# Kernel optimization log

Measured on AMD Instinct MI355X. Metric: run time of the kernel, lower is better.

The kernel has to match this reference:

```python
import jax, jax.numpy as jnp
import numpy as np

B, S, D = 2, 2048, 1024
H, DK = 16, 64


def setup_inputs() -> dict:
    key = jax.random.key(0)
    ks = jax.random.split(key, 10)
    scale = D ** -0.5
    x = jax.random.normal(ks[0], (B, S, D), dtype=jnp.float32)
    mask = jax.random.randint(ks[1], (B, S), 0, 2) > 0  # True = masked positions
    Wq = jax.random.normal(ks[2], (D, H * DK), dtype=jnp.float32) * scale
    Wk = jax.random.normal(ks[3], (D, H * DK), dtype=jnp.float32) * scale
    Wv = jax.random.normal(ks[4], (D, H * DK), dtype=jnp.float32) * scale
    Wo = jax.random.normal(ks[5], (H * DK, D), dtype=jnp.float32) * scale
    bq = jnp.zeros((H * DK,), jnp.float32)
    bk = jnp.zeros((H * DK,), jnp.float32)
    bv = jnp.zeros((H * DK,), jnp.float32)
    bo = jnp.zeros((D,), jnp.float32)
    return {"x": x, "mask": mask, "Wq": Wq, "bq": bq, "Wk": Wk, "bk": bk,
            "Wv": Wv, "bv": bv, "Wo": Wo, "bo": bo}


def reference(x, mask, Wq, bq, Wk, bk, Wv, bv, Wo, bo):
    b, s, _ = x.shape
    # Linear + activation (dropout is identity at eval)
    q = jax.nn.relu(x @ Wq + bq).reshape(b, s, H, DK)
    k = jax.nn.relu(x @ Wk + bk).reshape(b, s, H, DK)
    v = jax.nn.relu(x @ Wv + bv).reshape(b, s, H, DK)
    # scores: [B, H, Sq, Sk]
    attn = jnp.einsum("bqhd,bkhd->bhqk", q, k) * (DK ** -0.5)
    # NOTE: original uses masked_fill(mask, 1e-9) BEFORE softmax (not -inf)
    attn = jnp.where(mask[:, None, None, :], jnp.float32(1e-9), attn)
    attn = jax.nn.softmax(attn, axis=-1)
    out = jnp.einsum("bhqk,bkhd->bqhd", attn, v).reshape(b, s, H * DK)
    return jax.nn.relu(out @ Wo + bo)
```

## Files before the change

### kernel.cpp

```cpp
#include <hip/hip_runtime.h>
#include <stdint.h>

typedef __attribute__((ext_vector_type(8))) short short8;
typedef __attribute__((ext_vector_type(4))) short short4b;
typedef __attribute__((ext_vector_type(4))) float f32x4;
typedef __attribute__((ext_vector_type(4))) unsigned short ushort4_t;

#define MFMA16(a, b, c) __builtin_amdgcn_mfma_f32_16x16x32_bf16((a), (b), (c), 0, 0, 0)

#if defined(__HIP_DEVICE_COMPILE__)
  #if __has_builtin(__builtin_amdgcn_mfma_f32_16x16x16bf16_1k)
    #define MFMA16K16(a, b, c) __builtin_amdgcn_mfma_f32_16x16x16bf16_1k((a), (b), (c), 0, 0, 0)
  #else
    #define MFMA16K16(a, b, c) __builtin_amdgcn_mfma_f32_16x16x16_bf16((a), (b), (c), 0, 0, 0)
  #endif
#else
  #define MFMA16K16(a, b, c) (c)
#endif

#define SCL_F (0.125f * 1.44269504f)

__device__ __forceinline__ float b2f(unsigned short u) {
    union { unsigned u; float f; } c; c.u = ((unsigned)u) << 16; return c.f;
}
__device__ __forceinline__ unsigned short f2b(float f) {
    union { float f; unsigned u; } c; c.f = f;
    unsigned r = c.u + 0x7FFF + ((c.u >> 16) & 1);
    return (unsigned short)(r >> 16);
}
__device__ __forceinline__ unsigned f_as_u(float f) {
    union { float f; unsigned u; } c; c.f = f; return c.u;
}

__device__ __forceinline__ void g2lds16(const unsigned short* g, unsigned lds_byte_off) {
    __builtin_amdgcn_global_load_lds(
        (const __attribute__((address_space(1))) void*)(uintptr_t)g,
        (__attribute__((address_space(3))) void*)(uintptr_t)lds_byte_off,
        16, 0, 0);
}

__global__ void detect_dtype(const unsigned short* __restrict__ x, int* __restrict__ flag) {
    __shared__ int cnt;
    if (threadIdx.x == 0) cnt = 0;
    __syncthreads();
    int insane = 0;
    #pragma unroll
    for (int j = 0; j < 4; ++j) {
        unsigned short u = x[threadIdx.x * 4 + j];
        int e = (u >> 7) & 0xFF;
        if ((e >= 1 && e <= 90) || e >= 165) insane++;
    }
    atomicAdd(&cnt, insane);
    __syncthreads();
    if (threadIdx.x == 0) *flag = (cnt > 128) ? 1 : 0;
}

__global__ __launch_bounds__(256) void convtrans_k(const void* __restrict__ s0, const void* __restrict__ s1,
                                                   const void* __restrict__ s2, const void* __restrict__ s3,
                                                   const void* __restrict__ b0, const void* __restrict__ b1,
                                                   const void* __restrict__ b2, const void* __restrict__ b3s,
                                                   const void* __restrict__ xsrc,
                                                   unsigned short* __restrict__ xdst,
                                                   unsigned short* __restrict__ dstBase,
                                                   unsigned short* __restrict__ dstB3,
                                                   unsigned short* __restrict__ dstBo,
                                                   const int* __restrict__ flag) {
    const int z = blockIdx.z;
    if (z >= 5) {
        if (!*flag) return;
        const int slice = z - 5;
        const size_t i0 = (size_t)slice * 524288 + (blockIdx.y * 16 + blockIdx.x) * 2048 + threadIdx.x * 8;
        const float* s = (const float*)xsrc;
        float4 f0 = *(const float4*)&s[i0];
        float4 f1 = *(const float4*)&s[i0 + 4];
        unsigned short* t = &xdst[i0];
        t[0] = f2b(f0.x); t[1] = f2b(f0.y); t[2] = f2b(f0.z); t[3] = f2b(f0.w);
        t[4] = f2b(f1.x); t[5] = f2b(f1.y); t[6] = f2b(f1.z); t[7] = f2b(f1.w);
        return;
    }
    if (z == 4) {
        if (blockIdx.y != 0 || blockIdx.x >= 4) return;
        const int w = blockIdx.x;
        const void* src = (w == 0) ? b0 : (w == 1) ? b1 : (w == 2) ? b2 : b3s;
        const float bscl = (w == 0) ? SCL_F : 1.0f;
        #pragma unroll
        for (int j = 0; j < 4; ++j) {
            const int i = threadIdx.x * 4 + j;
            float fv = (*flag) ? ((const float*)src)[i] : b2f(((const unsigned short*)src)[i]);
            unsigned short v = f2b(fv * bscl);
            if (w < 3) dstB3[w * 1024 + i] = v;
            else dstBo[i] = v;
        }
        return;
    }
    __shared__ __align__(16) unsigned short tile[64 * 72];
    const void* src = (z == 0) ? s0 : (z == 1) ? s1 : (z == 2) ? s2 : s3;
    unsigned short* dst = dstBase + (size_t)z * 1024 * 1024;
    const float wscl = (z == 0) ? SCL_F : 1.0f;
    const int tid = threadIdx.x;
    const int r0 = blockIdx.y * 64, c0 = blockIdx.x * 64;
    const int rb = tid >> 3, c = (tid & 7) * 8;
    if (*flag) {
        const float* s = (const float*)src;
        #pragma unroll
        for (int it = 0; it < 2; ++it) {
            int rr = it * 32 + rb;
            float4 f0 = *(const float4*)&s[(size_t)(r0 + rr) * 1024 + c0 + c];
            float4 f1 = *(const float4*)&s[(size_t)(r0 + rr) * 1024 + c0 + c + 4];
            unsigned short* t = &tile[rr * 72 + c];
            t[0] = f2b(f0.x * wscl); t[1] = f2b(f0.y * wscl); t[2] = f2b(f0.z * wscl); t[3] = f2b(f0.w * wscl);
            t[4] = f2b(f1.x * wscl); t[5] = f2b(f1.y * wscl); t[6] = f2b(f1.z * wscl); t[7] = f2b(f1.w * wscl);
        }
    } else if (z == 0) {
        const unsigned short* s = (const unsigned short*)src;
        #pragma unroll
        for (int it = 0; it < 2; ++it) {
            int rr = it * 32 + rb;
            union { short8 v; unsigned short u[8]; } in;
            in.v = *(const short8*)&s[(size_t)(r0 + rr) * 1024 + c0 + c];
            unsigned short* t = &tile[rr * 72 + c];
            #pragma unroll
            for (int j = 0; j < 8; ++j) t[j] = f2b(b2f(in.u[j]) * SCL_F);
        }
    } else {
        const unsigned short* s = (const unsigned short*)src;
        #pragma unroll
        for (int it = 0; it < 2; ++it) {
            int rr = it * 32 + rb;
            *(short8*)&tile[rr * 72 + c] = *(const short8*)&s[(size_t)(r0 + rr) * 1024 + c0 + c];
        }
    }
    __syncthreads();
    #pragma unroll
    for (int it = 0; it < 2; ++it) {
        int n = it * 32 + rb, k8 = c;
        union { short8 s; unsigned short u[8]; } tmp;
        #pragma unroll
        for (int j = 0; j < 8; ++j) tmp.u[j] = tile[(k8 + j) * 72 + n];
        *(short8*)&dst[(size_t)(c0 + n) * 1024 + r0 + k8] = tmp.s;
    }
}

__global__ __launch_bounds__(256) void mask_k(unsigned short* __restrict__ qkv,
                                              const int* __restrict__ mask) {
    const int row = blockIdx.x * 2 + (threadIdx.x >> 7);
    const int col = (threadIdx.x & 127) * 8;
    if (mask[row]) {
        const short8 z = {0, 0, 0, 0, 0, 0, 0, 0};
        *(short8*)&qkv[(size_t)row * 3072 + 1024 + col] = z;
    }
}

__global__ __launch_bounds__(256) void gemm_bias_relu(const unsigned short* __restrict__ A,
                                                      const void* __restrict__ Araw,
                                                      const unsigned short* __restrict__ BT,
                                                      const unsigned short* __restrict__ bias,
                                                      void* __restrict__ C,
                                                      unsigned short* __restrict__ VtG,
                                                      const int* __restrict__ flag,
                                                      int M, int N, int K, int mode) {
    __shared__ __align__(16) unsigned short As[128 * 32];
    __shared__ __align__(16) unsigned short Bs[128 * 32];
    const int tid = threadIdx.x;
    const int wave = tid >> 6, lane = tid & 63;
    const int quad = lane >> 4, l16 = lane & 15;
    const int wm = wave >> 1, wn = wave & 1;
    const int m0 = blockIdx.y * 128, n0 = blockIdx.x * 128;

    const unsigned short* Ause = (Araw != nullptr && *flag == 0) ? (const unsigned short*)Araw : A;

    f32x4 acc[4][4];
    #pragma unroll
    for (int i = 0; i < 4; i++)
        #pragma unroll
        for (int j = 0; j < 4; j++) acc[i][j] = (f32x4){0.f, 0.f, 0.f, 0.f};

    const int srow = wave * 32 + (lane >> 2);
    const int sc8  = (lane & 3) * 8;
    const unsigned short* gA0 = Ause + (size_t)(m0 + srow) * K + sc8;
    const unsigned short* gA1 = gA0 + (size_t)16 * K;
    const unsigned short* gB0 = BT + (size_t)(n0 + srow) * K + sc8;
    const unsigned short* gB1 = gB0 + (size_t)16 * K;
    const unsigned ldsA = (unsigned)(uintptr_t)&As[0] + wave * 2048;
    const unsigned ldsB = (unsigned)(uintptr_t)&Bs[0] + wave * 2048;

    for (int k0 = 0; k0 < K; k0 += 32) {
        __syncthreads();
        g2lds16(gA0 + k0, ldsA);
        g2lds16(gA1 + k0, ldsA + 1024);
        g2lds16(gB0 + k0, ldsB);
        g2lds16(gB1 + k0, ldsB + 1024);
        __syncthreads();
        short8 af[4], bf[4];
        #pragma unroll
        for (int i = 0; i < 4; i++) af[i] = *(const short8*)&As[(wm * 64 + i * 16 + l16) * 32 + quad * 8];
        #pragma unroll
        for (int j = 0; j < 4; j++) bf[j] = *(const short8*)&Bs[(wn * 64 + j * 16 + l16) * 32 + quad * 8];
        #pragma unroll
        for (int i = 0; i < 4; i++)
            #pragma unroll
            for (int j = 0; j < 4; j++)
                acc[i][j] = MFMA16(af[i], bf[j], acc[i][j]);
    }

    if (mode == 2 && n0 >= 2048) {
        #pragma unroll
        for (int j = 0; j < 4; j++) {
            const int col = n0 + wn * 64 + j * 16 + l16;
            const int h  = (col - 2048) >> 6;
            const int dk = (col - 2048) & 63;
            const float bj = b2f(bias[col]);
            #pragma unroll
            for (int i = 0; i < 4; i++) {
                const int rowb = m0 + wm * 64 + i * 16 + quad * 4;
                const int bb = rowb >> 11;
                const int s0 = rowb & 2047;
                ushort4_t w;
                #pragma unroll
                for (int r = 0; r < 4; r++) {
                    float v = acc[i][j][r] + bj;
                    v = v > 0.f ? v : 0.f;
                    w[r] = f2b(v);
                }
                *(ushort4_t*)&VtG[(size_t)((bb * 16 + h) * 64 + dk) * 2048 + s0] = w;
            }
        }
    } else {
        const int f32out = (mode == 1) && (*flag != 0);
        #pragma unroll
        for (int j = 0; j < 4; j++) {
            const int col = n0 + wn * 64 + j * 16 + l16;
            const float bj = b2f(bias[col]);
            #pragma unroll
            for (int i = 0; i < 4; i++) {
                const int rowb = m0 + wm * 64 + i * 16 + quad * 4;
                #pragma unroll
                for (int r = 0; r < 4; r++) {
                    float v = acc[i][j][r] + bj;
                    v = v > 0.f ? v : 0.f;
                    if (f32out) ((float*)C)[(size_t)(rowb + r) * N + col] = v;
                    else ((unsigned short*)C)[(size_t)(rowb + r) * N + col] = f2b(v);
                }
            }
        }
    }
}

__global__ __launch_bounds__(256) void attn_kernel(const unsigned short* __restrict__ qkv,
                                                   const unsigned short* __restrict__ VtG,
                                                   unsigned short* __restrict__ out) {
    __shared__ __align__(16) unsigned short Ks[64 * 64];
    __shared__ __align__(16) unsigned short Vs[64 * 64];

    const int qt = blockIdx.x, bh = blockIdx.y;
    const int b = bh >> 4, h = bh & 15;
    const int tid = threadIdx.x, wave = tid >> 6, lane = tid & 63;
    const int quad = lane >> 4, l16 = lane & 15;

    const int qrowA = qt * 128 + wave * 16 + l16;
    const unsigned short* qpA = qkv + (size_t)(b * 2048 + qrowA) * 3072 + h * 64;
    const unsigned short* qpB = qpA + (size_t)64 * 3072;
    const short8 qa0 = *(const short8*)(qpA + quad * 8);
    const short8 qa1 = *(const short8*)(qpA + 32 + quad * 8);
    const short8 qb0 = *(const short8*)(qpB + quad * 8);
    const short8 qb1 = *(const short8*)(qpB + 32 + quad * 8);

    f32x4 oA[4], oB[4], sumA, sumB;
    #pragma unroll
    for (int n = 0; n < 4; n++) { oA[n] = (f32x4){0.f,0.f,0.f,0.f}; oB[n] = (f32x4){0.f,0.f,0.f,0.f}; }
    sumA = (f32x4){0.f,0.f,0.f,0.f};
    sumB = (f32x4){0.f,0.f,0.f,0.f};

    const short4b ones = { (short)0x3F80, (short)0x3F80, (short)0x3F80, (short)0x3F80 };

    const int srow = tid >> 2;
    const int scol = (tid & 3) * 16;
    const int sxor = (srow & 7) << 3;
    const unsigned short* kg = qkv + (size_t)(b * 2048 + srow) * 3072 + 1024 + h * 64 + scol;
    const unsigned short* vg = VtG + (size_t)(bh * 64 + srow) * 2048 + scol;
    const size_t kstep = (size_t)64 * 3072;
    unsigned short* wK0 = &Ks[(srow * 64 + scol) ^ sxor];
    unsigned short* wK1 = &Ks[(srow * 64 + scol + 8) ^ sxor];
    unsigned short* wV0 = &Vs[(srow * 64 + scol) ^ sxor];
    unsigned short* wV1 = &Vs[(srow * 64 + scol + 8) ^ sxor];

    const int rx = (l16 & 7) << 3;

    short8 rk0 = *(const short8*)(kg);
    short8 rk1 = *(const short8*)(kg + 8);
    short8 rv0 = *(const short8*)(vg);
    short8 rv1 = *(const short8*)(vg + 8);

    for (int kt = 0; kt < 32; ++kt) {
        __syncthreads();
        *(short8*)wK0 = rk0;
        *(short8*)wK1 = rk1;
        *(short8*)wV0 = rv0;
        *(short8*)wV1 = rv1;
        if (kt < 31) {
            rk0 = *(const short8*)(kg + (kt + 1) * kstep);
            rk1 = *(const short8*)(kg + (kt + 1) * kstep + 8);
            rv0 = *(const short8*)(vg + (kt + 1) * 64);
            rv1 = *(const short8*)(vg + (kt + 1) * 64 + 8);
        }
        __syncthreads();

        __builtin_amdgcn_s_setprio(1);
        f32x4 sA[4], sB[4];
        #pragma unroll
        for (int t = 0; t < 4; ++t) {
            const short8 kb0 = *(const short8*)&Ks[(((t * 16 + l16) * 64) + quad * 8) ^ rx];
            const short8 kb1 = *(const short8*)&Ks[(((t * 16 + l16) * 64) + 32 + quad * 8) ^ rx];
            f32x4 z = (f32x4){0.f, 0.f, 0.f, 0.f};
            sA[t] = MFMA16(kb1, qa1, MFMA16(kb0, qa0, z));
            sB[t] = MFMA16(kb1, qb1, MFMA16(kb0, qb0, z));
        }

        short4b vb[4][4];
        #pragma unroll
        for (int t = 0; t < 4; ++t)
            #pragma unroll
            for (int n = 0; n < 4; ++n)
                vb[t][n] = *(const short4b*)&Vs[(((n * 16 + l16) * 64) + t * 16 + quad * 4) ^ rx];

        #pragma unroll
        for (int t = 0; t < 4; ++t) {
            float pA[4], pB[4];
            #pragma unroll
            for (int r = 0; r < 4; ++r) {
                pA[r] = exp2f(sA[t][r]);
                pB[r] = exp2f(sB[t][r]);
            }
            union { unsigned u[2]; short4b s; } fa, fb;
            fa.u[0] = __builtin_amdgcn_perm(f_as_u(pA[1]), f_as_u(pA[0]), 0x07060302u);
            fa.u[1] = __builtin_amdgcn_perm(f_as_u(pA[3]), f_as_u(pA[2]), 0x07060302u);
            fb.u[0] = __builtin_amdgcn_perm(f_as_u(pB[1]), f_as_u(pB[0]), 0x07060302u);
            fb.u[1] = __builtin_amdgcn_perm(f_as_u(pB[3]), f_as_u(pB[2]), 0x07060302u);
            #pragma unroll
            for (int n = 0; n < 4; ++n) {
                oA[n] = MFMA16K16(fa.s, vb[t][n], oA[n]);
                oB[n] = MFMA16K16(fb.s, vb[t][n], oB[n]);
            }
            sumA = MFMA16K16(fa.s, ones, sumA);
            sumB = MFMA16K16(fb.s, ones, sumB);
        }
        __builtin_amdgcn_s_setprio(0);
    }

    float invA[4], invB[4];
    #pragma unroll
    for (int r = 0; r < 4; ++r) { invA[r] = 1.0f / sumA[r]; invB[r] = 1.0f / sumB[r]; }
    #pragma unroll
    for (int n = 0; n < 4; n++)
        #pragma unroll
        for (int r = 0; r < 4; r++) {
            const int row = qt * 128 + wave * 16 + quad * 4 + r;
            out[(size_t)(b * 2048 + row) * 1024 + h * 64 + n * 16 + l16] = f2b(oA[n][r] * invA[r]);
            out[(size_t)(b * 2048 + row + 64) * 1024 + h * 64 + n * 16 + l16] = f2b(oB[n][r] * invB[r]);
        }
}

extern "C" void kernel_launch(void* const* d_in, const int* in_sizes, int n_in,
                              void* d_out, int out_size, void* d_ws, size_t ws_size,
                              hipStream_t stream) {
    const void* x  = d_in[0];
    const int*  mk = (const int*)d_in[1];
    const void* Wq = d_in[2]; const void* bq = d_in[3];
    const void* Wk = d_in[4]; const void* bk = d_in[5];
    const void* Wv = d_in[6]; const void* bv = d_in[7];
    const void* Wo = d_in[8]; const void* bo = d_in[9];

    char* wsb = (char*)d_ws;
    int* flag = (int*)wsb;
    unsigned short* W0 = (unsigned short*)(wsb + 64);

    const size_t M1 = 1024u * 1024u;
    const size_t M4 = 4096u * 1024u;
    unsigned short* xb  = W0;
    unsigned short* WT  = xb + M4;
    unsigned short* WoT = WT + 3 * M1;
    unsigned short* b3  = WoT + M1;
    unsigned short* bob = b3 + 4096;
    unsigned short* qkv = bob + 1024;
    unsigned short* VtG = qkv + (size_t)4096 * 3072;
    unsigned short* abf = xb;

    detect_dtype<<<1, 256, 0, stream>>>((const unsigned short*)x, flag);

    convtrans_k<<<dim3(16, 16, 13), 256, 0, stream>>>(Wq, Wk, Wv, Wo, bq, bk, bv, bo,
                                                      x, xb, WT, b3, bob, flag);

    gemm_bias_relu<<<dim3(24, 32), 256, 0, stream>>>(xb, x, WT, b3, qkv, VtG, flag,
                                                     4096, 3072, 1024, 2);
    mask_k<<<2048, 256, 0, stream>>>(qkv, mk);
    attn_kernel<<<dim3(16, 32), 256, 0, stream>>>(qkv, VtG, abf);
    gemm_bias_relu<<<dim3(8, 32), 256, 0, stream>>>(abf, nullptr, WoT, bob, d_out, VtG, flag,
                                                    4096, 1024, 1024, 1);
}
```

Measured before the change: 227.2 us.

## Halve attention query tile and double-buffer K/V shared memory

The attention kernel now processes 64 query rows per block instead of 128 and launches twice as many blocks, giving 1024 workgroups instead of 512 to fill the GPU's compute units. K/V tiles are double-buffered in LDS, so each iteration needs one barrier instead of two, and the global loads for the next tile are issued two iterations ahead. The cost is that every K/V tile is loaded from global memory twice as many times overall, and LDS use per block doubles.

```diff
diff --git a/kernel.cpp b/kernel.cpp
--- a/kernel.cpp
+++ b/kernel.cpp
@@ -249,27 +249,23 @@
 __global__ __launch_bounds__(256) void attn_kernel(const unsigned short* __restrict__ qkv,
                                                    const unsigned short* __restrict__ VtG,
                                                    unsigned short* __restrict__ out) {
-    __shared__ __align__(16) unsigned short Ks[64 * 64];
-    __shared__ __align__(16) unsigned short Vs[64 * 64];
+    __shared__ __align__(16) unsigned short Ks[2][64 * 64];
+    __shared__ __align__(16) unsigned short Vs[2][64 * 64];
 
     const int qt = blockIdx.x, bh = blockIdx.y;
     const int b = bh >> 4, h = bh & 15;
     const int tid = threadIdx.x, wave = tid >> 6, lane = tid & 63;
     const int quad = lane >> 4, l16 = lane & 15;
 
-    const int qrowA = qt * 128 + wave * 16 + l16;
-    const unsigned short* qpA = qkv + (size_t)(b * 2048 + qrowA) * 3072 + h * 64;
-    const unsigned short* qpB = qpA + (size_t)64 * 3072;
-    const short8 qa0 = *(const short8*)(qpA + quad * 8);
-    const short8 qa1 = *(const short8*)(qpA + 32 + quad * 8);
-    const short8 qb0 = *(const short8*)(qpB + quad * 8);
-    const short8 qb1 = *(const short8*)(qpB + 32 + quad * 8);
-
-    f32x4 oA[4], oB[4], sumA, sumB;
-    #pragma unroll
-    for (int n = 0; n < 4; n++) { oA[n] = (f32x4){0.f,0.f,0.f,0.f}; oB[n] = (f32x4){0.f,0.f,0.f,0.f}; }
+    const int qrow = qt * 64 + wave * 16 + l16;
+    const unsigned short* qp = qkv + (size_t)(b * 2048 + qrow) * 3072 + h * 64;
+    const short8 qa0 = *(const short8*)(qp + quad * 8);
+    const short8 qa1 = *(const short8*)(qp + 32 + quad * 8);
+
+    f32x4 oA[4], sumA;
+    #pragma unroll
+    for (int n = 0; n < 4; n++) oA[n] = (f32x4){0.f,0.f,0.f,0.f};
     sumA = (f32x4){0.f,0.f,0.f,0.f};
-    sumB = (f32x4){0.f,0.f,0.f,0.f};
 
     const short4b ones = { (short)0x3F80, (short)0x3F80, (short)0x3F80, (short)0x3F80 };
 
@@ -279,41 +275,50 @@
     const unsigned short* kg = qkv + (size_t)(b * 2048 + srow) * 3072 + 1024 + h * 64 + scol;
     const unsigned short* vg = VtG + (size_t)(bh * 64 + srow) * 2048 + scol;
     const size_t kstep = (size_t)64 * 3072;
-    unsigned short* wK0 = &Ks[(srow * 64 + scol) ^ sxor];
-    unsigned short* wK1 = &Ks[(srow * 64 + scol + 8) ^ sxor];
-    unsigned short* wV0 = &Vs[(srow * 64 + scol) ^ sxor];
-    unsigned short* wV1 = &Vs[(srow * 64 + scol + 8) ^ sxor];
+    const int sidx0 = (srow * 64 + scol) ^ sxor;
+    const int sidx1 = (srow * 64 + scol + 8) ^ sxor;
 
     const int rx = (l16 & 7) << 3;
+
+    unsigned short* Ka = &Ks[0][0];  unsigned short* Kb = &Ks[1][0];
+    unsigned short* Va = &Vs[0][0];  unsigned short* Vb = &Vs[1][0];
 
     short8 rk0 = *(const short8*)(kg);
     short8 rk1 = *(const short8*)(kg + 8);
     short8 rv0 = *(const short8*)(vg);
     short8 rv1 = *(const short8*)(vg + 8);
+    *(short8*)(Ka + sidx0) = rk0;
+    *(short8*)(Ka + sidx1) = rk1;
+    *(short8*)(Va + sidx0) = rv0;
+    *(short8*)(Va + sidx1) = rv1;
+    rk0 = *(const short8*)(kg + kstep);
+    rk1 = *(const short8*)(kg + kstep + 8);
+    rv0 = *(const short8*)(vg + 64);
+    rv1 = *(const short8*)(vg + 64 + 8);
+    __syncthreads();
 
     for (int kt = 0; kt < 32; ++kt) {
-        __syncthreads();
-        *(short8*)wK0 = rk0;
-        *(short8*)wK1 = rk1;
-        *(short8*)wV0 = rv0;
-        *(short8*)wV1 = rv1;
         if (kt < 31) {
-            rk0 = *(const short8*)(kg + (kt + 1) * kstep);
-            rk1 = *(const short8*)(kg + (kt + 1) * kstep + 8);
-            rv0 = *(const short8*)(vg + (kt + 1) * 64);
-            rv1 = *(const short8*)(vg + (kt + 1) * 64 + 8);
-        }
-        __syncthreads();
+            *(short8*)(Kb + sidx0) = rk0;
+            *(short8*)(Kb + sidx1) = rk1;
+            *(short8*)(Vb + sidx0) = rv0;
+            *(short8*)(Vb + sidx1) = rv1;
+        }
+        if (kt < 30) {
+            rk0 = *(const short8*)(kg + (kt + 2) * kstep);
+            rk1 = *(const short8*)(kg + (kt + 2) * kstep + 8);
+            rv0 = *(const short8*)(vg + (kt + 2) * 64);
+            rv1 = *(const short8*)(vg + (kt + 2) * 64 + 8);
+        }
 
         __builtin_amdgcn_s_setprio(1);
-        f32x4 sA[4], sB[4];
+        f32x4 sA[4];
         #pragma unroll
         for (int t = 0; t < 4; ++t) {
-            const short8 kb0 = *(const short8*)&Ks[(((t * 16 + l16) * 64) + quad * 8) ^ rx];
-            const short8 kb1 = *(const short8*)&Ks[(((t * 16 + l16) * 64) + 32 + quad * 8) ^ rx];
+            const short8 kb0 = *(const short8*)&Ka[(((t * 16 + l16) * 64) + quad * 8) ^ rx];
+            const short8 kb1 = *(const short8*)&Ka[(((t * 16 + l16) * 64) + 32 + quad * 8) ^ rx];
             f32x4 z = (f32x4){0.f, 0.f, 0.f, 0.f};
             sA[t] = MFMA16(kb1, qa1, MFMA16(kb0, qa0, z));
-            sB[t] = MFMA16(kb1, qb1, MFMA16(kb0, qb0, z));
         }
 
         short4b vb[4][4];
@@ -321,42 +326,38 @@
         for (int t = 0; t < 4; ++t)
             #pragma unroll
             for (int n = 0; n < 4; ++n)
-                vb[t][n] = *(const short4b*)&Vs[(((n * 16 + l16) * 64) + t * 16 + quad * 4) ^ rx];
+                vb[t][n] = *(const short4b*)&Va[(((n * 16 + l16) * 64) + t * 16 + quad * 4) ^ rx];
 
         #pragma unroll
         for (int t = 0; t < 4; ++t) {
-            float pA[4], pB[4];
-            #pragma unroll
-            for (int r = 0; r < 4; ++r) {
-                pA[r] = exp2f(sA[t][r]);
-                pB[r] = exp2f(sB[t][r]);
-            }
-            union { unsigned u[2]; short4b s; } fa, fb;
+            float pA[4];
+            #pragma unroll
+            for (int r = 0; r < 4; ++r) pA[r] = exp2f(sA[t][r]);
+            union { unsigned u[2]; short4b s; } fa;
             fa.u[0] = __builtin_amdgcn_perm(f_as_u(pA[1]), f_as_u(pA[0]), 0x07060302u);
             fa.u[1] = __builtin_amdgcn_perm(f_as_u(pA[3]), f_as_u(pA[2]), 0x07060302u);
-            fb.u[0] = __builtin_amdgcn_perm(f_as_u(pB[1]), f_as_u(pB[0]), 0x07060302u);
-            fb.u[1] = __builtin_amdgcn_perm(f_as_u(pB[3]), f_as_u(pB[2]), 0x07060302u);
-            #pragma unroll
-            for (int n = 0; n < 4; ++n) {
+            #pragma unroll
+            for (int n = 0; n < 4; ++n)
                 oA[n] = MFMA16K16(fa.s, vb[t][n], oA[n]);
-                oB[n] = MFMA16K16(fb.s, vb[t][n], oB[n]);
-            }
             sumA = MFMA16K16(fa.s, ones, sumA);
-            sumB = MFMA16K16(fb.s, ones, sumB);
         }
         __builtin_amdgcn_s_setprio(0);
-    }
-
-    float invA[4], invB[4];
-    #pragma unroll
-    for (int r = 0; r < 4; ++r) { invA[r] = 1.0f / sumA[r]; invB[r] = 1.0f / sumB[r]; }
+        __syncthreads();
+
+        unsigned short* tp;
+        tp = Ka; Ka = Kb; Kb = tp;
+        tp = Va; Va = Vb; Vb = tp;
+    }
+
+    float invA[4];
+    #pragma unroll
+    for (int r = 0; r < 4; ++r) invA[r] = 1.0f / sumA[r];
     #pragma unroll
     for (int n = 0; n < 4; n++)
         #pragma unroll
         for (int r = 0; r < 4; r++) {
-            const int row = qt * 128 + wave * 16 + quad * 4 + r;
+            const int row = qt * 64 + wave * 16 + quad * 4 + r;
             out[(size_t)(b * 2048 + row) * 1024 + h * 64 + n * 16 + l16] = f2b(oA[n][r] * invA[r]);
-            out[(size_t)(b * 2048 + row + 64) * 1024 + h * 64 + n * 16 + l16] = f2b(oB[n][r] * invB[r]);
         }
 }
 
@@ -393,7 +394,7 @@
     gemm_bias_relu<<<dim3(24, 32), 256, 0, stream>>>(xb, x, WT, b3, qkv, VtG, flag,
                                                      4096, 3072, 1024, 2);
     mask_k<<<2048, 256, 0, stream>>>(qkv, mk);
-    attn_kernel<<<dim3(16, 32), 256, 0, stream>>>(qkv, VtG, abf);
+    attn_kernel<<<dim3(32, 32), 256, 0, stream>>>(qkv, VtG, abf);
     gemm_bias_relu<<<dim3(8, 32), 256, 0, stream>>>(abf, nullptr, WoT, bob, d_out, VtG, flag,
                                                     4096, 1024, 1024, 1);
 }
```

New measurement: 236.5 us. 1.04x slower.
